# Optimization experiments

Hardware: AMD Instinct MI355X
Metric: run time of the kernel (lower is better)

Reference implementation:

```python
import jax, jax.numpy as jnp
import numpy as np

# ---- config mirroring DetectionPostProcessV1 init + quant params ----
B, H, W, A, C = 8, 128, 128, 8, 8      # batch, feature HxW, anchors/cell, num_classes
STRIDE = 8
IMG_W, IMG_H = 1024, 1024               # image_size
INPUT_SHIFT = 4                          # kInputShift -> in_scale = 1/16
EXP_SHIFT = 4                            # from _gen_exp_table with in_scale 1/16
BOX_THR_INT = 9                          # ceil(0.55 * 2**INPUT_SHIFT)
NMS_THR = 128.0 / 256.0                  # ceil(0.5 * 2**kNmsThresholdShift) / 2**8
NMS_MARGIN = 0.0                         # nms_margin (quantized: ceil(0*16)/16)
PRE_K, POST_K = 1024, 300                # pre-NMS candidates, post_nms_top_k
CLASS_OFFSETS = jnp.zeros((C,), jnp.int32)
CLASS_SEP = 4096.0                       # coordinate offset for class-aware NMS


def setup_inputs() -> dict:
    key = jax.random.key(0)
    k1, _ = jax.random.split(key)
    # int8 repr of quantized head outputs (stored as int32 for jax indexing)
    data = jax.random.randint(k1, (B, A * (4 + C), H, W), -128, 128, dtype=jnp.int32)
    # grid anchors: 8 sizes per cell, stride-8 feature map
    sizes = np.array([16, 24, 32, 48, 64, 96, 128, 192], np.float32)
    ys = (np.arange(H, dtype=np.float32) + 0.5) * STRIDE
    xs = (np.arange(W, dtype=np.float32) + 0.5) * STRIDE
    cy, cx = np.meshgrid(ys, xs, indexing="ij")
    cx, cy = cx[..., None], cy[..., None]              # [H,W,1]
    w = np.broadcast_to(sizes, (H, W, A))
    h = np.broadcast_to(sizes, (H, W, A))
    anchors = np.stack([cx - w / 2, cy - h / 2, cx + w / 2, cy + h / 2], -1)
    anchors = jnp.asarray(anchors.reshape(-1, 4).astype(np.float32))  # [N,4] matches [H,W,A] flatten order
    # integer exp table, exactly as _gen_exp_table
    in_scale = 1.0 / (1 << INPUT_SHIFT)
    idx = np.arange(-128, 128, dtype=np.float32) * in_scale
    ev = np.exp(idx)
    exp_table = jnp.asarray(np.round(ev * (1 << EXP_SHIFT)).astype(np.int32))
    return {"data": data, "anchors": anchors, "exp_table": exp_table}


def _post_process(data, anchors, exp_table):
    N = H * W * A
    # [B, A*(4+C), H, W] -> [B, N, 4+C]
    x = data.reshape(B, A, 4 + C, H, W).transpose(0, 3, 4, 1, 2).reshape(B, N, 4 + C)
    box_d = x[..., :4]
    scores_i = x[..., 4:] + CLASS_OFFSETS                      # int scores with class offsets
    # decode: dx,dy via fixed-point shift; dw,dh via int exp table lookup
    dxy = box_d[..., :2].astype(jnp.float32) / (1 << INPUT_SHIFT)
    expv = exp_table[box_d[..., 2:4] + 128].astype(jnp.float32) / (1 << EXP_SHIFT)
    ctr = (anchors[:, :2] + anchors[:, 2:]) * 0.5              # [N,2]
    wh = anchors[:, 2:] - anchors[:, :2]
    pc = ctr + dxy * wh                                        # [B,N,2]
    pwh = wh * expv
    boxes = jnp.concatenate([pc - pwh * 0.5, pc + pwh * 0.5], -1)
    boxes = jnp.clip(boxes, 0.0, jnp.array([IMG_W, IMG_H, IMG_W, IMG_H], jnp.float32))
    # score filter
    best = scores_i.max(-1)
    label = scores_i.argmax(-1).astype(jnp.int32)
    valid = best >= BOX_THR_INT
    score = best.astype(jnp.float32) / (1 << INPUT_SHIFT)
    sc_masked = jnp.where(valid, score, -1e9)
    topv, topi = jax.lax.top_k(sc_masked, PRE_K)               # [B,PRE_K]
    bk = jnp.take_along_axis(boxes, topi[..., None], 1)        # [B,PRE_K,4]
    lk = jnp.take_along_axis(label, topi, 1)
    vk = topv > -1e8
    # class-aware NMS via coordinate offset trick
    ob = bk + lk[..., None].astype(jnp.float32) * CLASS_SEP
    area = (ob[..., 2] - ob[..., 0]) * (ob[..., 3] - ob[..., 1])
    lt = jnp.maximum(ob[:, :, None, :2], ob[:, None, :, :2])
    rb = jnp.minimum(ob[:, :, None, 2:], ob[:, None, :, 2:])
    whi = jnp.clip(rb - lt, 0.0)
    inter = whi[..., 0] * whi[..., 1]
    iou = inter / (area[:, :, None] + area[:, None, :] - inter + 1e-9)  # [B,PRE_K,PRE_K]
    idxr = jnp.arange(PRE_K)

    def body(i, sup):
        alive_i = ~jnp.take(sup, i, axis=1)                    # [B]
        iou_i = jnp.take(iou, i, axis=1)                       # [B,PRE_K]
        s_i = jnp.take(topv, i, axis=1)[:, None]
        cond = (alive_i[:, None] & (iou_i > NMS_THR)
                & (topv <= s_i - NMS_MARGIN) & (idxr > i)[None, :])
        return sup | cond

    sup = jax.lax.fori_loop(0, PRE_K, body, ~vk)
    keep = vk & ~sup
    fs = jnp.where(keep, topv, -1e9)
    outv, outi = jax.lax.top_k(fs, POST_K)
    boxes_out = jnp.take_along_axis(bk, outi[..., None], 1)
    labels = jnp.take_along_axis(lk, outi, 1)
    ok = outv > -1e8
    boxes_out = jnp.where(ok[..., None], boxes_out, 0.0)       # [B,POST_K,4]
    scores_out = jnp.where(ok, outv, 0.0)                      # [B,POST_K]
    labels_out = jnp.where(ok, labels, -1)                     # [B,POST_K]
    return boxes_out, scores_out, labels_out


def reference(data, anchors, exp_table):
    return _post_process(data, anchors, exp_table)
```

## Files before the change

### kernel.cpp

```cpp
#include <hip/hip_runtime.h>
#include <stdint.h>

#define Bb 8
#define PREK 1024
#define POSTK 300
#define NBIN 120
#define NCHUNK 512

__device__ __forceinline__ float clampb(float v){ return fminf(fmaxf(v, 0.0f), 1024.0f); }

__global__ void __launch_bounds__(256) k1_scores(const int* __restrict__ data,
                                                 unsigned short* __restrict__ sc16,
                                                 int* __restrict__ chist){
    int blk = blockIdx.x;
    int b = blk >> 7, h = blk & 127;
    int tid = threadIdx.x;
    int a = tid >> 5, wg = tid & 31;
    int w = wg << 2;
    const int* p = data + (((size_t)(b*96 + a*12 + 4)) << 14) + (h << 7) + w;
    int4 m = *(const int4*)p;
    int4 lb = make_int4(0,0,0,0);
#pragma unroll
    for (int c = 1; c < 8; ++c){
        int4 v = *(const int4*)(p + ((size_t)c << 14));
        if (v.x > m.x){ m.x = v.x; lb.x = c; }
        if (v.y > m.y){ m.y = v.y; lb.y = c; }
        if (v.z > m.z){ m.z = v.z; lb.z = c; }
        if (v.w > m.w){ m.w = v.w; lb.w = c; }
    }
    ushort4 st;
    st.x = (unsigned short)(((m.x + 128) << 8) | lb.x);
    st.y = (unsigned short)(((m.y + 128) << 8) | lb.y);
    st.z = (unsigned short)(((m.z + 128) << 8) | lb.z);
    st.w = (unsigned short)(((m.w + 128) << 8) | lb.w);
    *(ushort4*)(sc16 + (((size_t)(b*8 + a)) << 14) + (h << 7) + w) = st;

    __shared__ int hist[4][NBIN];
    for (int i = tid; i < 4*NBIN; i += 256) ((int*)hist)[i] = 0;
    __syncthreads();
    int q = wg >> 3;
    if (m.x >= 9) atomicAdd(&hist[q][m.x-9], 1);
    if (m.y >= 9) atomicAdd(&hist[q][m.y-9], 1);
    if (m.z >= 9) atomicAdd(&hist[q][m.z-9], 1);
    if (m.w >= 9) atomicAdd(&hist[q][m.w-9], 1);
    __syncthreads();
    int* cb = chist + ((size_t)(b*NCHUNK + h*4)) * NBIN;
    for (int i = tid; i < 4*NBIN; i += 256) cb[i] = ((int*)hist)[i];
}

__global__ void __launch_bounds__(256) k2_select(int* __restrict__ chist, int* __restrict__ gt,
                                                 int* __restrict__ Tb_, int* __restrict__ dmeta){
    int b = blockIdx.x, tid = threadIdx.x;
    __shared__ int hs2[2][NBIN];
    __shared__ int suf[128];
    __shared__ int Tsh;
    __shared__ int sb[512];
    if (tid == 0) Tsh = -1;
    int half = tid >> 7, bin = tid & 127;
    const int* cb = chist + (size_t)b * NCHUNK * NBIN;
    if (bin < NBIN){
        int s = 0;
        const int* p2 = cb + (size_t)half*256*NBIN + bin;
#pragma unroll 8
        for (int ch = 0; ch < 256; ++ch) s += p2[(size_t)ch * NBIN];
        hs2[half][bin] = s;
    }
    __syncthreads();
    int hbin = 0;
    if (tid < 128){
        hbin = (tid < NBIN) ? hs2[0][tid] + hs2[1][tid] : 0;
        suf[tid] = hbin;
    }
    __syncthreads();
    for (int off = 1; off < 128; off <<= 1){
        int v = 0;
        if (tid < 128 && tid + off < 128) v = suf[tid + off];
        __syncthreads();
        if (tid < 128) suf[tid] += v;
        __syncthreads();
    }
    if (tid < NBIN){
        gt[b*128 + tid] = suf[tid] - hbin;
        if (suf[tid] >= PREK) atomicMax(&Tsh, tid);
    }
    __syncthreads();
    int T = Tsh > 0 ? Tsh : 0;
    if (tid == 0) Tb_[b] = T;
    for (int k = tid; k < PREK; k += 256) dmeta[b*PREK + k] = -1;
    int i0 = tid, i1 = tid + 256;
    for (int abin = T; abin < NBIN; ++abin){
        int* basep = chist + (size_t)(b*NCHUNK) * NBIN + abin;
        int v0 = basep[(size_t)i0 * NBIN], v1 = basep[(size_t)i1 * NBIN];
        sb[i0] = v0; sb[i1] = v1;
        __syncthreads();
        for (int off = 1; off < 512; off <<= 1){
            int a0 = (i0 >= off) ? sb[i0 - off] : 0;
            int a1 = (i1 >= off) ? sb[i1 - off] : 0;
            __syncthreads();
            sb[i0] += a0; sb[i1] += a1;
            __syncthreads();
        }
        basep[(size_t)i0 * NBIN] = sb[i0] - v0;
        basep[(size_t)i1 * NBIN] = sb[i1] - v1;
        __syncthreads();
    }
}

__global__ void __launch_bounds__(256) k3_rank(const unsigned short* __restrict__ sc16,
                                               const int* __restrict__ chist,
                                               const int* __restrict__ gt, const int* __restrict__ Tb_,
                                               const int* __restrict__ data,
                                               const float* __restrict__ anchors,
                                               const int* __restrict__ etab,
                                               float4* __restrict__ dbox, int* __restrict__ dmeta){
    int blk = blockIdx.x;
    int b = blk >> 9, ci = blk & 511;
    int tid = threadIdx.x;
    int h = ci >> 2, w0 = (ci & 3) << 5;
    __shared__ unsigned short sc[256];
    __shared__ int wcnt[4][NBIN];
    if (tid < 64){
        int a = tid & 7, wq = tid >> 3;
        ushort4 v4 = *(const ushort4*)(sc16 + (((size_t)(b*8 + a)) << 14) + (h << 7) + w0 + (wq << 2));
        sc[(wq*4 + 0)*8 + a] = v4.x;
        sc[(wq*4 + 1)*8 + a] = v4.y;
        sc[(wq*4 + 2)*8 + a] = v4.z;
        sc[(wq*4 + 3)*8 + a] = v4.w;
    }
    for (int i = tid; i < 4*NBIN; i += 256) ((int*)wcnt)[i] = 0;
    int T = Tb_[b];
    __syncthreads();
    unsigned short v = sc[tid];
    int s = (int)(v >> 8) - 128;
    int bin = s - 9;
    bool qual = (bin >= T);
    int wv = tid >> 6, lane = tid & 63;
    if (qual) atomicAdd(&wcnt[wv][bin], 1);
    __syncthreads();
    int myeq = 0;
    {
        unsigned long long low = (1ull << lane) - 1ull;
        for (int vb = T; vb < NBIN; ++vb){
            unsigned long long bal = __ballot(qual && bin == vb);
            if (!bal) continue;
            if (qual && bin == vb) myeq = __popcll(bal & low);
        }
    }
    if (!qual) return;
    int cross = 0;
    for (int w2 = 0; w2 < wv; ++w2) cross += wcnt[w2][bin];
    int rank = gt[b*128 + bin] + chist[((size_t)(b*NCHUNK) + ci)*NBIN + bin] + cross + myeq;
    if (rank < PREK){
        int n = ci*256 + tid;
        int a = n & 7, wc = (n >> 3) & 127;
        const int* p = data + (((size_t)(b*96 + a*12)) << 14) + (h << 7) + wc;
        int d0 = p[0], d1 = p[1 << 14], d2 = p[2 << 14], d3 = p[3 << 14];
        float4 an = ((const float4*)anchors)[n];
        float cx = __fmul_rn(__fadd_rn(an.x, an.z), 0.5f);
        float cy = __fmul_rn(__fadd_rn(an.y, an.w), 0.5f);
        float wx = __fsub_rn(an.z, an.x), wy = __fsub_rn(an.w, an.y);
        float dx = __fmul_rn((float)d0, 0.0625f), dy = __fmul_rn((float)d1, 0.0625f);
        float ex = __fmul_rn((float)etab[d2 + 128], 0.0625f);
        float ey = __fmul_rn((float)etab[d3 + 128], 0.0625f);
        float pcx = __fadd_rn(cx, __fmul_rn(dx, wx));
        float pcy = __fadd_rn(cy, __fmul_rn(dy, wy));
        float hx = __fmul_rn(__fmul_rn(wx, ex), 0.5f);
        float hy = __fmul_rn(__fmul_rn(wy, ey), 0.5f);
        float x1 = clampb(__fsub_rn(pcx, hx)), y1 = clampb(__fsub_rn(pcy, hy));
        float x2 = clampb(__fadd_rn(pcx, hx)), y2 = clampb(__fadd_rn(pcy, hy));
        dbox[b*PREK + rank] = make_float4(x1, y1, x2, y2);
        dmeta[b*PREK + rank] = (int)v;
    }
}

__global__ void __launch_bounds__(1024) k45_nms_out(const float4* __restrict__ dbox,
                                                    const int* __restrict__ dmeta,
                                                    float* __restrict__ out){
    int b = blockIdx.x, tid = threadIdx.x, lane = tid & 63, wv = tid >> 6;
    __shared__ float X1[1024], Y1[1024], X2[1024], Y2[1024], AR[1024];
    __shared__ unsigned long long MAT[1024][4];
    __shared__ unsigned char KEEP[1024];
    __shared__ int wq[16][8];
    __shared__ int cbs[8], ccn[8];
    __shared__ int wcn[16];
    __shared__ int totS;

    int v = dmeta[b*PREK + tid];
    float4 bb = dbox[b*PREK + tid];
    bool valid = (v >= 0);
    int lc = valid ? (v & 255) : -1;
    float sval = valid ? __fmul_rn((float)((v >> 8) - 128), 0.0625f) : 0.0f;
    int win = 0;
#pragma unroll
    for (int c = 0; c < 8; ++c){
        unsigned long long bal = __ballot(lc == c);
        if (lane == 0) wq[wv][c] = __popcll(bal);
        if (lc == c) win = __popcll(bal & ((1ull << lane) - 1ull));
    }
    __syncthreads();
    if (tid < 8){
        int run = 0;
        for (int w2 = 0; w2 < 16; ++w2){ int t = wq[w2][tid]; wq[w2][tid] = run; run += t; }
        ccn[tid] = run;
    }
    __syncthreads();
    if (tid == 0){
        int run = 0;
        for (int c = 0; c < 8; ++c){ cbs[c] = run; run += ccn[c]; }
    }
    __syncthreads();
    int p = 0;
    if (valid){
        p = cbs[lc] + wq[wv][lc] + win;
        float off = (float)(lc << 12);
        float ox1 = __fadd_rn(bb.x, off), oy1 = __fadd_rn(bb.y, off);
        float ox2 = __fadd_rn(bb.z, off), oy2 = __fadd_rn(bb.w, off);
        X1[p] = ox1; Y1[p] = oy1; X2[p] = ox2; Y2[p] = oy2;
        AR[p] = __fmul_rn(__fsub_rn(ox2, ox1), __fsub_rn(oy2, oy1));
    }
    __syncthreads();

    if (wv < 8){
        int M = ccn[wv], base = cbs[wv];
        if (M > 0){
            if (M <= 256){
                float cx1[4], cy1[4], cx2[4], cy2[4], ca[4];
#pragma unroll
                for (int g = 0; g < 4; ++g){
                    int j = g*64 + lane;
                    int ad = base + ((j < M) ? j : 0);
                    cx1[g]=X1[ad]; cy1[g]=Y1[ad]; cx2[g]=X2[ad]; cy2[g]=Y2[ad]; ca[g]=AR[ad];
                }
                for (int i = 0; i < M; ++i){
                    float xi1 = X1[base+i], yi1 = Y1[base+i];
                    float xi2 = X2[base+i], yi2 = Y2[base+i], ai = AR[base+i];
#pragma unroll
                    for (int g = 0; g < 4; ++g){
                        if (g*64 < M){
                            unsigned long long bal = 0;
                            if ((g+1)*64 > i){
                                bool o = false;
                                int j = g*64 + lane;
                                if (j < M && j > i){
                                    float wx = fmaxf(__fsub_rn(fminf(xi2, cx2[g]), fmaxf(xi1, cx1[g])), 0.0f);
                                    float wy = fmaxf(__fsub_rn(fminf(yi2, cy2[g]), fmaxf(yi1, cy1[g])), 0.0f);
                                    float inter = __fmul_rn(wx, wy);
                                    float den = __fadd_rn(__fsub_rn(__fadd_rn(ai, ca[g]), inter), 1e-9f);
                                    o = (__fdiv_rn(inter, den) > 0.5f);
                                }
                                bal = __ballot(o);
                            }
                            if (lane == 0) MAT[base+i][g] = bal;
                        }
                    }
                }
                unsigned long long rem0=0, rem1=0, rem2=0, rem3=0;
                unsigned long long c0 = MAT[base][0], c1 = MAT[base][1];
                unsigned long long c2 = MAT[base][2], c3 = MAT[base][3];
                for (int i = 0; i < M; ++i){
                    unsigned long long r0=c0, r1=c1, r2=c2, r3=c3;
                    int inx = (i+1 < M) ? i+1 : i;
                    c0 = MAT[base+inx][0]; c1 = MAT[base+inx][1];
                    c2 = MAT[base+inx][2]; c3 = MAT[base+inx][3];
                    int s = i >> 6;
                    unsigned long long rs = (s==0) ? rem0 : (s==1) ? rem1 : (s==2) ? rem2 : rem3;
                    if (!((rs >> (i & 63)) & 1ull)){
                        rem0 |= r0; rem1 |= r1; rem2 |= r2; rem3 |= r3;
                    }
                }
                {
                    int j0 = lane;
                    if (j0       < M) KEEP[base+j0]       = (unsigned char)(((rem0 >> lane) & 1ull) ^ 1ull);
                    if (j0 + 64  < M) KEEP[base+j0+64]    = (unsigned char)(((rem1 >> lane) & 1ull) ^ 1ull);
                    if (j0 + 128 < M) KEEP[base+j0+128]   = (unsigned char)(((rem2 >> lane) & 1ull) ^ 1ull);
                    if (j0 + 192 < M) KEEP[base+j0+192]   = (unsigned char)(((rem3 >> lane) & 1ull) ^ 1ull);
                }
            } else {
                for (int m = lane; m < M; m += 64) KEEP[base+m] = 0;
                for (int i = 0; i < M; ++i){
                    if (KEEP[base+i]) continue;
                    float xi1 = X1[base+i], yi1 = Y1[base+i];
                    float xi2 = X2[base+i], yi2 = Y2[base+i], ai = AR[base+i];
                    for (int j = i + 1 + lane; j < M; j += 64){
                        if (KEEP[base+j]) continue;
                        float wx = fmaxf(__fsub_rn(fminf(xi2, X2[base+j]), fmaxf(xi1, X1[base+j])), 0.0f);
                        float wy = fmaxf(__fsub_rn(fminf(yi2, Y2[base+j]), fmaxf(yi1, Y1[base+j])), 0.0f);
                        float inter = __fmul_rn(wx, wy);
                        float den = __fadd_rn(__fsub_rn(__fadd_rn(ai, AR[base+j]), inter), 1e-9f);
                        if (__fdiv_rn(inter, den) > 0.5f) KEEP[base+j] = 1;
                    }
                }
                for (int m = lane; m < M; m += 64) KEEP[base+m] ^= 1;
            }
        }
    }
    __syncthreads();

    bool kp = valid && (KEEP[p] != 0);
    unsigned long long bal = __ballot(kp);
    if (lane == 0) wcn[wv] = __popcll(bal);
    __syncthreads();
    if (tid == 0){
        int r = 0;
        for (int w2 = 0; w2 < 16; ++w2){ int t = wcn[w2]; wcn[w2] = r; r += t; }
        totS = r;
    }
    __syncthreads();
    int pos = wcn[wv] + __popcll(bal & ((1ull << lane) - 1ull));
    float* boxes  = out;
    float* scores = out + Bb*POSTK*4;
    float* labs   = out + Bb*POSTK*5;
    if (kp && pos < POSTK){
        int o = (b*POSTK + pos)*4;
        boxes[o+0] = bb.x; boxes[o+1] = bb.y; boxes[o+2] = bb.z; boxes[o+3] = bb.w;
        scores[b*POSTK + pos] = sval;
        labs[b*POSTK + pos] = (float)lc;
    }
    int tot = totS < POSTK ? totS : POSTK;
    if (tid >= tot && tid < POSTK){
        int o = (b*POSTK + tid)*4;
        boxes[o+0] = 0.f; boxes[o+1] = 0.f; boxes[o+2] = 0.f; boxes[o+3] = 0.f;
        scores[b*POSTK + tid] = 0.f;
        labs[b*POSTK + tid] = -1.0f;
    }
}

extern "C" void kernel_launch(void* const* d_in, const int* in_sizes, int n_in,
                              void* d_out, int out_size, void* d_ws, size_t ws_size,
                              hipStream_t stream) {
    const int*   data    = (const int*)d_in[0];
    const float* anchors = (const float*)d_in[1];
    const int*   etab    = (const int*)d_in[2];
    float* out = (float*)d_out;

    char* ws = (char*)d_ws;
    size_t off = 0;
    auto alloc = [&](size_t bytes)->char*{ char* p = ws + off; off += (bytes + 255) & ~(size_t)255; return p; };
    unsigned short* sc16 = (unsigned short*)alloc((size_t)Bb*8*16384*2);
    int* chist           = (int*)alloc((size_t)Bb*NCHUNK*NBIN*4);
    int* gt              = (int*)alloc((size_t)Bb*128*4);
    int* Tb_             = (int*)alloc((size_t)Bb*4);
    float4* dbox         = (float4*)alloc((size_t)Bb*PREK*16);
    int* dmeta           = (int*)alloc((size_t)Bb*PREK*4);
    (void)ws_size; (void)in_sizes; (void)n_in; (void)out_size;

    k1_scores<<<Bb*128, 256, 0, stream>>>(data, sc16, chist);
    k2_select<<<Bb, 256, 0, stream>>>(chist, gt, Tb_, dmeta);
    k3_rank<<<Bb*NCHUNK, 256, 0, stream>>>(sc16, chist, gt, Tb_, data, anchors, etab, dbox, dmeta);
    k45_nms_out<<<Bb, 1024, 0, stream>>>(dbox, dmeta, out);
}
```

Baseline: 178.3 us.

## Keep NMS suppression bitmask in registers and resolve it with wave shuffles

The per-class NMS no longer builds a 1024x4 u64 suppression matrix in shared memory. Each lane now owns up to four rows and builds their column bitmasks in registers by looping over columns j, which are broadcast from LDS. The serial resolve pass then pulls rows with __shfl instead of reading LDS. This removes 32KB of LDS and the per-row ballot/store traffic. In exchange it evaluates the full MxM IoU matrix rather than the upper triangle, uses a 16-register u64 mask array, and adds shuffle latency inside the serial loop.

```diff
diff --git a/kernel.cpp b/kernel.cpp
--- a/kernel.cpp
+++ b/kernel.cpp
@@ -178,7 +178,6 @@
                                                     float* __restrict__ out){
     int b = blockIdx.x, tid = threadIdx.x, lane = tid & 63, wv = tid >> 6;
     __shared__ float X1[1024], Y1[1024], X2[1024], Y2[1024], AR[1024];
-    __shared__ unsigned long long MAT[1024][4];
     __shared__ unsigned char KEEP[1024];
     __shared__ int wq[16][8];
     __shared__ int cbs[8], ccn[8];
@@ -190,6 +189,7 @@
     bool valid = (v >= 0);
     int lc = valid ? (v & 255) : -1;
     float sval = valid ? __fmul_rn((float)((v >> 8) - 128), 0.0625f) : 0.0f;
+    KEEP[tid] = 0;
     int win = 0;
 #pragma unroll
     for (int c = 0; c < 8; ++c){
@@ -222,76 +222,83 @@
 
     if (wv < 8){
         int M = ccn[wv], base = cbs[wv];
-        if (M > 0){
-            if (M <= 256){
-                float cx1[4], cy1[4], cx2[4], cy2[4], ca[4];
-#pragma unroll
-                for (int g = 0; g < 4; ++g){
-                    int j = g*64 + lane;
-                    int ad = base + ((j < M) ? j : 0);
-                    cx1[g]=X1[ad]; cy1[g]=Y1[ad]; cx2[g]=X2[ad]; cy2[g]=Y2[ad]; ca[g]=AR[ad];
-                }
-                for (int i = 0; i < M; ++i){
-                    float xi1 = X1[base+i], yi1 = Y1[base+i];
-                    float xi2 = X2[base+i], yi2 = Y2[base+i], ai = AR[base+i];
-#pragma unroll
-                    for (int g = 0; g < 4; ++g){
-                        if (g*64 < M){
-                            unsigned long long bal = 0;
-                            if ((g+1)*64 > i){
-                                bool o = false;
-                                int j = g*64 + lane;
-                                if (j < M && j > i){
-                                    float wx = fmaxf(__fsub_rn(fminf(xi2, cx2[g]), fmaxf(xi1, cx1[g])), 0.0f);
-                                    float wy = fmaxf(__fsub_rn(fminf(yi2, cy2[g]), fmaxf(yi1, cy1[g])), 0.0f);
-                                    float inter = __fmul_rn(wx, wy);
-                                    float den = __fadd_rn(__fsub_rn(__fadd_rn(ai, ca[g]), inter), 1e-9f);
-                                    o = (__fdiv_rn(inter, den) > 0.5f);
-                                }
-                                bal = __ballot(o);
+        if (M > 0 && M <= 256){
+            float rx1[4], ry1[4], rx2[4], ry2[4], rar[4];
+#pragma unroll
+            for (int g = 0; g < 4; ++g){
+                int r = g*64 + lane;
+                int ad = base + ((r < M) ? r : 0);
+                rx1[g]=X1[ad]; ry1[g]=Y1[ad]; rx2[g]=X2[ad]; ry2[g]=Y2[ad]; rar[g]=AR[ad];
+            }
+            unsigned long long mk[4][4];
+#pragma unroll
+            for (int g = 0; g < 4; ++g)
+#pragma unroll
+                for (int w2 = 0; w2 < 4; ++w2) mk[g][w2] = 0ull;
+
+#pragma unroll
+            for (int jw = 0; jw < 4; ++jw){
+                if (jw*64 < M){
+                    int lim = M - jw*64; if (lim > 64) lim = 64;
+                    for (int jl = 0; jl < lim; ++jl){
+                        int j = jw*64 + jl;
+                        int aj = base + j;
+                        float jx1 = X1[aj], jy1 = Y1[aj], jx2 = X2[aj], jy2 = Y2[aj], jar = AR[aj];
+#pragma unroll
+                        for (int g = 0; g < 4; ++g){
+                            if (g*64 < M){
+                                int i = g*64 + lane;
+                                float wx = fmaxf(__fsub_rn(fminf(rx2[g], jx2), fmaxf(rx1[g], jx1)), 0.0f);
+                                float wy = fmaxf(__fsub_rn(fminf(ry2[g], jy2), fmaxf(ry1[g], jy1)), 0.0f);
+                                float inter = __fmul_rn(wx, wy);
+                                float den = __fadd_rn(__fsub_rn(__fadd_rn(rar[g], jar), inter), 1e-9f);
+                                bool o = (__fdiv_rn(inter, den) > 0.5f) && (j > i);
+                                mk[g][jw] |= o ? (1ull << jl) : 0ull;
                             }
-                            if (lane == 0) MAT[base+i][g] = bal;
                         }
                     }
                 }
-                unsigned long long rem0=0, rem1=0, rem2=0, rem3=0;
-                unsigned long long c0 = MAT[base][0], c1 = MAT[base][1];
-                unsigned long long c2 = MAT[base][2], c3 = MAT[base][3];
-                for (int i = 0; i < M; ++i){
-                    unsigned long long r0=c0, r1=c1, r2=c2, r3=c3;
-                    int inx = (i+1 < M) ? i+1 : i;
-                    c0 = MAT[base+inx][0]; c1 = MAT[base+inx][1];
-                    c2 = MAT[base+inx][2]; c3 = MAT[base+inx][3];
-                    int s = i >> 6;
-                    unsigned long long rs = (s==0) ? rem0 : (s==1) ? rem1 : (s==2) ? rem2 : rem3;
-                    if (!((rs >> (i & 63)) & 1ull)){
-                        rem0 |= r0; rem1 |= r1; rem2 |= r2; rem3 |= r3;
+            }
+
+            unsigned long long r0=0ull, r1=0ull, r2=0ull, r3=0ull;
+#pragma unroll
+            for (int iw = 0; iw < 4; ++iw){
+                if (iw*64 < M){
+                    int lim = M - iw*64; if (lim > 64) lim = 64;
+                    for (int il = 0; il < lim; ++il){
+                        unsigned long long cur = (iw==0)?r0:(iw==1)?r1:(iw==2)?r2:r3;
+                        if (!((cur >> il) & 1ull)){
+                            unsigned long long w0 = __shfl(mk[iw][0], il);
+                            unsigned long long w1 = __shfl(mk[iw][1], il);
+                            unsigned long long w2_ = __shfl(mk[iw][2], il);
+                            unsigned long long w3_ = __shfl(mk[iw][3], il);
+                            r0 |= w0; r1 |= w1; r2 |= w2_; r3 |= w3_;
+                        }
                     }
                 }
-                {
-                    int j0 = lane;
-                    if (j0       < M) KEEP[base+j0]       = (unsigned char)(((rem0 >> lane) & 1ull) ^ 1ull);
-                    if (j0 + 64  < M) KEEP[base+j0+64]    = (unsigned char)(((rem1 >> lane) & 1ull) ^ 1ull);
-                    if (j0 + 128 < M) KEEP[base+j0+128]   = (unsigned char)(((rem2 >> lane) & 1ull) ^ 1ull);
-                    if (j0 + 192 < M) KEEP[base+j0+192]   = (unsigned char)(((rem3 >> lane) & 1ull) ^ 1ull);
+            }
+#pragma unroll
+            for (int g = 0; g < 4; ++g){
+                int r = g*64 + lane;
+                unsigned long long rg = (g==0)?r0:(g==1)?r1:(g==2)?r2:r3;
+                if (r < M) KEEP[base + r] = (unsigned char)(((rg >> lane) & 1ull) ^ 1ull);
+            }
+        } else if (M > 256){
+            for (int m = lane; m < M; m += 64) KEEP[base+m] = 0;
+            for (int i = 0; i < M; ++i){
+                if (KEEP[base+i]) continue;
+                float xi1 = X1[base+i], yi1 = Y1[base+i];
+                float xi2 = X2[base+i], yi2 = Y2[base+i], ai = AR[base+i];
+                for (int j = i + 1 + lane; j < M; j += 64){
+                    if (KEEP[base+j]) continue;
+                    float wx = fmaxf(__fsub_rn(fminf(xi2, X2[base+j]), fmaxf(xi1, X1[base+j])), 0.0f);
+                    float wy = fmaxf(__fsub_rn(fminf(yi2, Y2[base+j]), fmaxf(yi1, Y1[base+j])), 0.0f);
+                    float inter = __fmul_rn(wx, wy);
+                    float den = __fadd_rn(__fsub_rn(__fadd_rn(ai, AR[base+j]), inter), 1e-9f);
+                    if (__fdiv_rn(inter, den) > 0.5f) KEEP[base+j] = 1;
                 }
-            } else {
-                for (int m = lane; m < M; m += 64) KEEP[base+m] = 0;
-                for (int i = 0; i < M; ++i){
-                    if (KEEP[base+i]) continue;
-                    float xi1 = X1[base+i], yi1 = Y1[base+i];
-                    float xi2 = X2[base+i], yi2 = Y2[base+i], ai = AR[base+i];
-                    for (int j = i + 1 + lane; j < M; j += 64){
-                        if (KEEP[base+j]) continue;
-                        float wx = fmaxf(__fsub_rn(fminf(xi2, X2[base+j]), fmaxf(xi1, X1[base+j])), 0.0f);
-                        float wy = fmaxf(__fsub_rn(fminf(yi2, Y2[base+j]), fmaxf(yi1, Y1[base+j])), 0.0f);
-                        float inter = __fmul_rn(wx, wy);
-                        float den = __fadd_rn(__fsub_rn(__fadd_rn(ai, AR[base+j]), inter), 1e-9f);
-                        if (__fdiv_rn(inter, den) > 0.5f) KEEP[base+j] = 1;
-                    }
-                }
-                for (int m = lane; m < M; m += 64) KEEP[base+m] ^= 1;
-            }
+            }
+            for (int m = lane; m < M; m += 64) KEEP[base+m] ^= 1;
         }
     }
     __syncthreads();
```

Measured after the change: 153.3 us. 14.0% less time.
